# Kernel optimization log

Hardware: AMD Instinct MI355X
Metric: run time of the kernel (lower is better)

The kernel has to match this reference:

```python
import jax, jax.numpy as jnp
import numpy as np

P = 256          # planes == in_planes
EPS = 1e-5       # BatchNorm eps


def binarize(x):
    # sign with sign(0) -> +1, as in standard binary-net quantizers
    return jnp.where(x >= 0, 1.0, -1.0).astype(x.dtype)


def bin_conv(x, w, stride=1):
    """XNOR-style binarized 3x3 conv: sign(x) * sign(w), scaled by per-out-channel mean |w|."""
    ba = binarize(x)
    bw = binarize(w)
    scale = jnp.mean(jnp.abs(w), axis=(1, 2, 3))  # [O]
    y = jax.lax.conv_general_dilated(
        ba, bw, window_strides=(stride, stride), padding=((1, 1), (1, 1)),
        dimension_numbers=("NCHW", "OIHW", "NCHW"))
    return y * scale[None, :, None, None]


def bn(x, gamma, beta, mean, var):
    # inference-mode BatchNorm2d
    inv = gamma / jnp.sqrt(var + EPS)
    return x * inv[None, :, None, None] + (beta - mean * inv)[None, :, None, None]


def channel_shuffle(x, groups=2):
    b, c, h, w = x.shape
    return x.reshape(b, groups, c // groups, h, w).transpose(0, 2, 1, 3, 4).reshape(b, c, h, w)


def setup_inputs() -> dict:
    key = jax.random.key(0)
    ks = jax.random.split(key, 8)
    B, H, W = 16, 56, 56
    return {
        "x": jax.random.normal(ks[0], (B, 2 * P, H, W), jnp.float32),
        "w1": jax.random.normal(ks[1], (P, P, 3, 3), jnp.float32) * 0.05,
        "w2": jax.random.normal(ks[2], (P, 2 * P, 3, 3), jnp.float32) * 0.05,
        "gamma1": jnp.ones((P,), jnp.float32),
        "beta1": jnp.zeros((P,), jnp.float32),
        "mean1": jax.random.normal(ks[3], (P,), jnp.float32) * 0.1,
        "var1": jax.random.uniform(ks[4], (P,), jnp.float32) + 0.5,
        "gamma2": jnp.ones((P,), jnp.float32),
        "beta2": jnp.zeros((P,), jnp.float32),
        "mean2": jax.random.normal(ks[5], (P,), jnp.float32) * 0.1,
        "var2": jax.random.uniform(ks[6], (P,), jnp.float32) + 0.5,
        "move_bias": jax.random.normal(ks[7], (1, P, 1, 1), jnp.float32) * 0.1,
    }


def reference(x, w1, w2, gamma1, beta1, mean1, var1,
              gamma2, beta2, mean2, var2, move_bias):
    x_act, x_idle = x[:, :P], x[:, P:]
    residual = x_act
    out = bn(bin_conv(x_act, w1, stride=1), gamma1, beta1, mean1, var1)
    out = out + residual
    out = jnp.clip(out, -1.0, 1.0)            # Hardtanh
    x_idle = x_idle + move_bias               # LearnableBias
    out = jnp.concatenate([out, x_idle], axis=1)   # [B, 2P, H, W]
    out = channel_shuffle(out, groups=2)
    residual1 = out[:, :P]
    out = bn(bin_conv(out, w2, stride=1), gamma2, beta2, mean2, var2)
    out = out + residual1
    out = jnp.clip(out, -1.0, 1.0)            # Hardtanh
    return out
```

## Files before the change

### kernel.cpp

```cpp
#include <hip/hip_runtime.h>
#include <cstdint>

typedef unsigned long long u64;
typedef unsigned short u16;

#define HWSZ 3136
#define WD 56
#define NPIX 50176

__device__ __forceinline__ float clampf(float v){ return fminf(1.0f, fmaxf(-1.0f, v)); }

__global__ __launch_bounds__(256) void k_wprep(
    const float* __restrict__ w1, const float* __restrict__ w2,
    const float* __restrict__ g1, const float* __restrict__ be1,
    const float* __restrict__ m1, const float* __restrict__ v1,
    const float* __restrict__ g2, const float* __restrict__ be2,
    const float* __restrict__ m2, const float* __restrict__ v2,
    u64* __restrict__ w1b, u64* __restrict__ w2e, u64* __restrict__ w2o,
    float* __restrict__ A1, float* __restrict__ B1,
    float* __restrict__ A2, float* __restrict__ B2)
{
    int co  = blockIdx.x;
    int tid = threadIdx.x;
    int wv = tid >> 6, lane = tid & 63;
    int ci = (wv << 6) + lane;

    float s1 = 0.f, s2 = 0.f;
    const float* w1p = w1 + ((size_t)co * 256 + ci) * 9;
#pragma unroll
    for (int t = 0; t < 9; t++) {
        float v = w1p[t];
        s1 += fabsf(v);
        u64 bal = __ballot(v >= 0.f);
        if (lane == 0) w1b[(co * 9 + t) * 4 + wv] = bal;
    }
    const float* wep = w2 + ((size_t)co * 512 + 2 * ci) * 9;
    const float* wop = wep + 9;
#pragma unroll
    for (int t = 0; t < 9; t++) {
        float ve = wep[t], vo = wop[t];
        s2 += fabsf(ve) + fabsf(vo);
        u64 bale = __ballot(ve >= 0.f);
        u64 balo = __ballot(vo >= 0.f);
        if (lane == 0) { w2e[(co * 9 + t) * 4 + wv] = bale; w2o[(co * 9 + t) * 4 + wv] = balo; }
    }
    __shared__ float red1[256], red2[256];
    red1[tid] = s1; red2[tid] = s2;
    __syncthreads();
    for (int off = 128; off > 0; off >>= 1) {
        if (tid < off) { red1[tid] += red1[tid + off]; red2[tid] += red2[tid + off]; }
        __syncthreads();
    }
    if (tid == 0) {
        float scale1 = red1[0] / 2304.f;
        float scale2 = red2[0] / 4608.f;
        float inv1 = g1[co] / sqrtf(v1[co] + 1e-5f);
        float inv2 = g2[co] / sqrtf(v2[co] + 1e-5f);
        A1[co] = scale1 * inv1;  B1[co] = be1[co] - m1[co] * inv1;
        A2[co] = scale2 * inv2;  B2[co] = be2[co] - m2[co] * inv2;
    }
}

__global__ __launch_bounds__(256) void k_pack(
    const float* __restrict__ x, const float* __restrict__ mb,
    u64* __restrict__ bitsA, u64* __restrict__ bitsI)
{
    int tid = threadIdx.x;
    int p = blockIdx.x * 256 + tid;
    int q = blockIdx.y;
    int b = p / HWSZ, hw = p % HWSZ;
    const float* xa = x + ((size_t)(b * 512 + q * 64)) * HWSZ + hw;
    const float* xi = x + ((size_t)(b * 512 + 256 + q * 64)) * HWSZ + hw;
    const float* mbq = mb + q * 64;
    u64 wa = 0, wi = 0;
#pragma unroll 8
    for (int j = 0; j < 64; j++) {
        float va = xa[(size_t)j * HWSZ];
        float vi = xi[(size_t)j * HWSZ] + mbq[j];
        wa |= (u64)(va >= 0.f) << j;
        wi |= (u64)(vi >= 0.f) << j;
    }
    bitsA[(size_t)p * 4 + q] = wa;
    bitsI[(size_t)p * 4 + q] = wi;
}

__global__ __launch_bounds__(256, 4) void k_conv1(
    const float* __restrict__ x, const u64* __restrict__ bitsA,
    const u64* __restrict__ w1b, const float* __restrict__ A1, const float* __restrict__ B1,
    u64* __restrict__ bitsC, float* __restrict__ c1v)
{
    __shared__ u64 sw[2304];
    __shared__ float sA[64], sB[64];
    __shared__ u16 spart[4][128];
    int tid = threadIdx.x;
    int q = blockIdx.y;
    int cobase = q * 64;
    {
        const u64* src = w1b + (size_t)cobase * 36;
#pragma unroll
        for (int i = 0; i < 9; i++) sw[tid + i * 256] = src[tid + i * 256];
        if (tid < 64) { sA[tid] = A1[cobase + tid]; sB[tid] = B1[cobase + tid]; }
    }
    __syncthreads();

    int g = tid >> 6, lane = tid & 63;
    int pix0 = blockIdx.x * 128 + lane * 2;
    int b = pix0 / HWSZ, hw = pix0 % HWSZ;
    int h = hw / WD, w = hw % WD;

    int acc[16][2];
#pragma unroll
    for (int co = 0; co < 16; co++) { acc[co][0] = 0; acc[co][1] = 0; }
    int nv0 = 0, nv1 = 0;

#pragma unroll 1
    for (int dy = -1; dy <= 1; dy++) {
        bool rowok = ((unsigned)(h + dy)) < (unsigned)WD;
        u64 cb[4][4];
        int m[4];
#pragma unroll
        for (int k = 0; k < 4; k++) {
            int c = w - 1 + k;
            bool ok = rowok && ((unsigned)c < (unsigned)WD);
            int pg = pix0 + dy * WD + (k - 1);
            pg = pg < 0 ? 0 : (pg > NPIX - 1 ? NPIX - 1 : pg);
            const ulonglong2* pb = (const ulonglong2*)(bitsA + (size_t)pg * 4);
            ulonglong2 b01 = pb[0], b23 = pb[1];
            cb[k][0] = b01.x; cb[k][1] = b01.y; cb[k][2] = b23.x; cb[k][3] = b23.y;
            m[k] = ok ? -1 : 0;
        }
        int tbase = (dy + 1) * 3;
#pragma unroll
        for (int dx = 0; dx < 3; dx++) {
            int t = tbase + dx;
            nv0 -= m[dx]; nv1 -= m[dx + 1];
#pragma unroll
            for (int co = 0; co < 16; co++) {
                const u64* wp = &sw[(((g << 4) + co) * 9 + t) * 4];
                u64 w0 = wp[0], w1_ = wp[1], w2_ = wp[2], w3_ = wp[3];
#pragma unroll
                for (int p = 0; p < 2; p++) {
                    int k = dx + p;
                    int pt = __popcll(cb[k][0] ^ w0) + __popcll(cb[k][1] ^ w1_)
                           + __popcll(cb[k][2] ^ w2_) + __popcll(cb[k][3] ^ w3_);
                    acc[co][p] += pt & m[k];
                }
            }
        }
    }

    unsigned sb0 = 0, sb1 = 0;
    bool wr = (q < 2);
#pragma unroll
    for (int co = 0; co < 16; co++) {
        int col = (g << 4) + co;
        int coG = cobase + col;
        float A = sA[col], B = sB[col];
        float2 xr = *(const float2*)(x + (size_t)(b * 512 + coG) * HWSZ + hw);
        float v0 = (float)((nv0 << 8) - 2 * acc[co][0]) * A + B + xr.x;
        float v1 = (float)((nv1 << 8) - 2 * acc[co][1]) * A + B + xr.y;
        sb0 |= (unsigned)(v0 >= 0.f) << co;
        sb1 |= (unsigned)(v1 >= 0.f) << co;
        if (wr) {
            *(float2*)(c1v + (size_t)coG * NPIX + pix0) = make_float2(clampf(v0), clampf(v1));
        }
    }
    spart[g][lane * 2]     = (u16)sb0;
    spart[g][lane * 2 + 1] = (u16)sb1;
    __syncthreads();
    if (g == 0) {
#pragma unroll
        for (int p = 0; p < 2; p++) {
            int pi = lane * 2 + p;
            u64 word = (u64)spart[0][pi] | ((u64)spart[1][pi] << 16)
                     | ((u64)spart[2][pi] << 32) | ((u64)spart[3][pi] << 48);
            bitsC[(size_t)(pix0 + p) * 4 + q] = word;
        }
    }
}

__global__ __launch_bounds__(256, 3) void k_conv2(
    const float* __restrict__ x, const float* __restrict__ mb,
    const u64* __restrict__ bitsC, const u64* __restrict__ bitsI,
    const u64* __restrict__ w2e, const u64* __restrict__ w2o,
    const float* __restrict__ A2, const float* __restrict__ B2,
    const float* __restrict__ c1v, float* __restrict__ out)
{
    __shared__ u64 se[2304], so[2304];
    __shared__ float sA[64], sB[64], sM[32];
    int tid = threadIdx.x;
    int q = blockIdx.y;
    int cobase = q * 64;
    {
        const u64* srcE = w2e + (size_t)cobase * 36;
        const u64* srcO = w2o + (size_t)cobase * 36;
#pragma unroll
        for (int i = 0; i < 9; i++) { se[tid + i * 256] = srcE[tid + i * 256]; so[tid + i * 256] = srcO[tid + i * 256]; }
        if (tid < 64) { sA[tid] = A2[cobase + tid]; sB[tid] = B2[cobase + tid]; }
        if (tid < 32) { sM[tid] = mb[q * 32 + tid]; }
    }
    __syncthreads();

    int g = tid >> 6, lane = tid & 63;
    int pix0 = blockIdx.x * 128 + lane * 2;
    int b = pix0 / HWSZ, hw = pix0 % HWSZ;
    int h = hw / WD, w = hw % WD;

    int acc[16][2];
#pragma unroll
    for (int co = 0; co < 16; co++) { acc[co][0] = 0; acc[co][1] = 0; }
    int nv0 = 0, nv1 = 0;

#pragma unroll 1
    for (int dy = -1; dy <= 1; dy++) {
        bool rowok = ((unsigned)(h + dy)) < (unsigned)WD;
        u64 cb[4][4], ib[4][4];
        int m[4];
#pragma unroll
        for (int k = 0; k < 4; k++) {
            int c = w - 1 + k;
            bool ok = rowok && ((unsigned)c < (unsigned)WD);
            int pg = pix0 + dy * WD + (k - 1);
            pg = pg < 0 ? 0 : (pg > NPIX - 1 ? NPIX - 1 : pg);
            const ulonglong2* pc = (const ulonglong2*)(bitsC + (size_t)pg * 4);
            const ulonglong2* pi = (const ulonglong2*)(bitsI + (size_t)pg * 4);
            ulonglong2 c01 = pc[0], c23 = pc[1];
            ulonglong2 i01 = pi[0], i23 = pi[1];
            cb[k][0] = c01.x; cb[k][1] = c01.y; cb[k][2] = c23.x; cb[k][3] = c23.y;
            ib[k][0] = i01.x; ib[k][1] = i01.y; ib[k][2] = i23.x; ib[k][3] = i23.y;
            m[k] = ok ? -1 : 0;
        }
        int tbase = (dy + 1) * 3;
#pragma unroll
        for (int dx = 0; dx < 3; dx++) {
            int t = tbase + dx;
            nv0 -= m[dx]; nv1 -= m[dx + 1];
#pragma unroll
            for (int co = 0; co < 16; co++) {
                const u64* we = &se[(((g << 4) + co) * 9 + t) * 4];
                const u64* wo = &so[(((g << 4) + co) * 9 + t) * 4];
                u64 e0 = we[0], e1 = we[1], e2 = we[2], e3 = we[3];
                u64 o0 = wo[0], o1 = wo[1], o2 = wo[2], o3 = wo[3];
#pragma unroll
                for (int p = 0; p < 2; p++) {
                    int k = dx + p;
                    int pt = __popcll(cb[k][0] ^ e0) + __popcll(cb[k][1] ^ e1)
                           + __popcll(cb[k][2] ^ e2) + __popcll(cb[k][3] ^ e3)
                           + __popcll(ib[k][0] ^ o0) + __popcll(ib[k][1] ^ o1)
                           + __popcll(ib[k][2] ^ o2) + __popcll(ib[k][3] ^ o3);
                    acc[co][p] += pt & m[k];
                }
            }
        }
    }

#pragma unroll
    for (int co = 0; co < 16; co++) {
        int col = (g << 4) + co;
        int coG = cobase + col;
        int cg2 = coG >> 1;
        float A = sA[col], B = sB[col];
        float v0 = (float)((nv0 << 9) - 2 * acc[co][0]) * A + B;
        float v1 = (float)((nv1 << 9) - 2 * acc[co][1]) * A + B;
        float r0, r1;
        if ((co & 1) == 0) {
            float2 cv = *(const float2*)(c1v + (size_t)cg2 * NPIX + pix0);
            r0 = cv.x; r1 = cv.y;
        } else {
            float2 xi = *(const float2*)(x + (size_t)(b * 512 + 256 + cg2) * HWSZ + hw);
            float mbv = sM[col >> 1];
            r0 = xi.x + mbv; r1 = xi.y + mbv;
        }
        *(float2*)(out + (size_t)(b * 256 + coG) * HWSZ + hw) =
            make_float2(clampf(v0 + r0), clampf(v1 + r1));
    }
}

extern "C" void kernel_launch(void* const* d_in, const int* in_sizes, int n_in,
                              void* d_out, int out_size, void* d_ws, size_t ws_size,
                              hipStream_t stream)
{
    const float* x   = (const float*)d_in[0];
    const float* w1  = (const float*)d_in[1];
    const float* w2  = (const float*)d_in[2];
    const float* g1  = (const float*)d_in[3];
    const float* be1 = (const float*)d_in[4];
    const float* m1  = (const float*)d_in[5];
    const float* v1  = (const float*)d_in[6];
    const float* g2  = (const float*)d_in[7];
    const float* be2 = (const float*)d_in[8];
    const float* m2  = (const float*)d_in[9];
    const float* v2  = (const float*)d_in[10];
    const float* mb  = (const float*)d_in[11];

    char* ws = (char*)d_ws;
    u64* w1b = (u64*)ws; ws += 73728;
    u64* w2e = (u64*)ws; ws += 73728;
    u64* w2o = (u64*)ws; ws += 73728;
    float* A1 = (float*)ws; ws += 1024;
    float* B1 = (float*)ws; ws += 1024;
    float* A2 = (float*)ws; ws += 1024;
    float* B2 = (float*)ws; ws += 1024;
    u64* bitsA = (u64*)ws; ws += (size_t)NPIX * 4 * 8;
    u64* bitsI = (u64*)ws; ws += (size_t)NPIX * 4 * 8;
    u64* bitsC = (u64*)ws; ws += (size_t)NPIX * 4 * 8;
    float* c1v = (float*)ws; ws += (size_t)128 * NPIX * 4;

    hipLaunchKernelGGL(k_wprep, dim3(256), dim3(256), 0, stream,
                       w1, w2, g1, be1, m1, v1, g2, be2, m2, v2,
                       w1b, w2e, w2o, A1, B1, A2, B2);
    hipLaunchKernelGGL(k_pack, dim3(196, 4), dim3(256), 0, stream, x, mb, bitsA, bitsI);
    hipLaunchKernelGGL(k_conv1, dim3(392, 4), dim3(256), 0, stream,
                       x, bitsA, w1b, A1, B1, bitsC, c1v);
    hipLaunchKernelGGL(k_conv2, dim3(392, 4), dim3(256), 0, stream,
                       x, mb, bitsC, bitsI, w2e, w2o, A2, B2, c1v, (float*)d_out);
}
```

Before: 409.8 us.

## Process four pixels per thread in binary convs and store intermediate as bf16

Each thread now computes four adjacent output pixels instead of two, so the six loaded neighbour bit-words and each shared-memory weight load are reused across more popcounts, and the grid halves. Conv2 splits its active and idle halves into two sequential passes to limit register pressure, and the valid-tap counts are computed in closed form. The clamped conv1 residual buffer is written and read as bf16 instead of fp32, halving that traffic but adding rounding error to the residual. Occupancy hint for conv1 drops from 4 to 3 waves per SIMD, and the larger accumulator arrays raise register use.

```diff
diff --git a/kernel.cpp b/kernel.cpp
--- a/kernel.cpp
+++ b/kernel.cpp
@@ -9,6 +9,11 @@
 #define NPIX 50176
 
 __device__ __forceinline__ float clampf(float v){ return fminf(1.0f, fmaxf(-1.0f, v)); }
+__device__ __forceinline__ u16 f2bf(float f){
+    unsigned u = __float_as_uint(f);
+    return (u16)((u + 0x7fffu + ((u >> 16) & 1u)) >> 16);
+}
+__device__ __forceinline__ float bf2f(u16 h){ return __uint_as_float(((unsigned)h) << 16); }
 
 __global__ __launch_bounds__(256) void k_wprep(
     const float* __restrict__ w1, const float* __restrict__ w2,
@@ -84,14 +89,14 @@
     bitsI[(size_t)p * 4 + q] = wi;
 }
 
-__global__ __launch_bounds__(256, 4) void k_conv1(
+__global__ __launch_bounds__(256, 3) void k_conv1(
     const float* __restrict__ x, const u64* __restrict__ bitsA,
     const u64* __restrict__ w1b, const float* __restrict__ A1, const float* __restrict__ B1,
-    u64* __restrict__ bitsC, float* __restrict__ c1v)
+    u64* __restrict__ bitsC, u16* __restrict__ c1v)
 {
     __shared__ u64 sw[2304];
     __shared__ float sA[64], sB[64];
-    __shared__ u16 spart[4][128];
+    __shared__ u16 spart[4][256];
     int tid = threadIdx.x;
     int q = blockIdx.y;
     int cobase = q * 64;
@@ -104,74 +109,89 @@
     __syncthreads();
 
     int g = tid >> 6, lane = tid & 63;
-    int pix0 = blockIdx.x * 128 + lane * 2;
+    int pix0 = blockIdx.x * 256 + lane * 4;
     int b = pix0 / HWSZ, hw = pix0 % HWSZ;
     int h = hw / WD, w = hw % WD;
 
-    int acc[16][2];
-#pragma unroll
-    for (int co = 0; co < 16; co++) { acc[co][0] = 0; acc[co][1] = 0; }
-    int nv0 = 0, nv1 = 0;
+    int acc[16][4];
+#pragma unroll
+    for (int co = 0; co < 16; co++)
+#pragma unroll
+        for (int p = 0; p < 4; p++) acc[co][p] = 0;
 
 #pragma unroll 1
     for (int dy = -1; dy <= 1; dy++) {
         bool rowok = ((unsigned)(h + dy)) < (unsigned)WD;
-        u64 cb[4][4];
-        int m[4];
-#pragma unroll
-        for (int k = 0; k < 4; k++) {
+        u64 pos[6][4];
+        int m[6];
+#pragma unroll
+        for (int k = 0; k < 6; k++) {
             int c = w - 1 + k;
             bool ok = rowok && ((unsigned)c < (unsigned)WD);
             int pg = pix0 + dy * WD + (k - 1);
             pg = pg < 0 ? 0 : (pg > NPIX - 1 ? NPIX - 1 : pg);
             const ulonglong2* pb = (const ulonglong2*)(bitsA + (size_t)pg * 4);
-            ulonglong2 b01 = pb[0], b23 = pb[1];
-            cb[k][0] = b01.x; cb[k][1] = b01.y; cb[k][2] = b23.x; cb[k][3] = b23.y;
+            ulonglong2 a01 = pb[0], a23 = pb[1];
+            pos[k][0] = a01.x; pos[k][1] = a01.y; pos[k][2] = a23.x; pos[k][3] = a23.y;
             m[k] = ok ? -1 : 0;
         }
         int tbase = (dy + 1) * 3;
 #pragma unroll
         for (int dx = 0; dx < 3; dx++) {
             int t = tbase + dx;
-            nv0 -= m[dx]; nv1 -= m[dx + 1];
 #pragma unroll
             for (int co = 0; co < 16; co++) {
                 const u64* wp = &sw[(((g << 4) + co) * 9 + t) * 4];
                 u64 w0 = wp[0], w1_ = wp[1], w2_ = wp[2], w3_ = wp[3];
 #pragma unroll
-                for (int p = 0; p < 2; p++) {
+                for (int p = 0; p < 4; p++) {
                     int k = dx + p;
-                    int pt = __popcll(cb[k][0] ^ w0) + __popcll(cb[k][1] ^ w1_)
-                           + __popcll(cb[k][2] ^ w2_) + __popcll(cb[k][3] ^ w3_);
+                    int pt = __popcll(pos[k][0] ^ w0) + __popcll(pos[k][1] ^ w1_)
+                           + __popcll(pos[k][2] ^ w2_) + __popcll(pos[k][3] ^ w3_);
                     acc[co][p] += pt & m[k];
                 }
             }
         }
     }
 
-    unsigned sb0 = 0, sb1 = 0;
+    int rowsv = 3 - (h == 0) - (h == WD - 1);
+    int nv[4];
+#pragma unroll
+    for (int p = 0; p < 4; p++) {
+        int wp_ = w + p;
+        nv[p] = rowsv * (3 - (wp_ == 0) - (wp_ == WD - 1));
+    }
+
+    unsigned sb[4] = {0, 0, 0, 0};
     bool wr = (q < 2);
 #pragma unroll
     for (int co = 0; co < 16; co++) {
         int col = (g << 4) + co;
         int coG = cobase + col;
         float A = sA[col], B = sB[col];
-        float2 xr = *(const float2*)(x + (size_t)(b * 512 + coG) * HWSZ + hw);
-        float v0 = (float)((nv0 << 8) - 2 * acc[co][0]) * A + B + xr.x;
-        float v1 = (float)((nv1 << 8) - 2 * acc[co][1]) * A + B + xr.y;
-        sb0 |= (unsigned)(v0 >= 0.f) << co;
-        sb1 |= (unsigned)(v1 >= 0.f) << co;
+        float4 xr = *(const float4*)(x + (size_t)(b * 512 + coG) * HWSZ + hw);
+        float v0 = (float)((nv[0] << 8) - 2 * acc[co][0]) * A + B + xr.x;
+        float v1 = (float)((nv[1] << 8) - 2 * acc[co][1]) * A + B + xr.y;
+        float v2 = (float)((nv[2] << 8) - 2 * acc[co][2]) * A + B + xr.z;
+        float v3 = (float)((nv[3] << 8) - 2 * acc[co][3]) * A + B + xr.w;
+        sb[0] |= (unsigned)(v0 >= 0.f) << co;
+        sb[1] |= (unsigned)(v1 >= 0.f) << co;
+        sb[2] |= (unsigned)(v2 >= 0.f) << co;
+        sb[3] |= (unsigned)(v3 >= 0.f) << co;
         if (wr) {
-            *(float2*)(c1v + (size_t)coG * NPIX + pix0) = make_float2(clampf(v0), clampf(v1));
-        }
-    }
-    spart[g][lane * 2]     = (u16)sb0;
-    spart[g][lane * 2 + 1] = (u16)sb1;
+            ushort4 st;
+            st.x = f2bf(clampf(v0)); st.y = f2bf(clampf(v1));
+            st.z = f2bf(clampf(v2)); st.w = f2bf(clampf(v3));
+            *(ushort4*)(c1v + (size_t)coG * NPIX + pix0) = st;
+        }
+    }
+#pragma unroll
+    for (int p = 0; p < 4; p++) spart[g][lane * 4 + p] = (u16)sb[p];
     __syncthreads();
     if (g == 0) {
 #pragma unroll
-        for (int p = 0; p < 2; p++) {
-            int pi = lane * 2 + p;
+        for (int p = 0; p < 4; p++) {
+            int pi = lane * 4 + p;
             u64 word = (u64)spart[0][pi] | ((u64)spart[1][pi] << 16)
                      | ((u64)spart[2][pi] << 32) | ((u64)spart[3][pi] << 48);
             bitsC[(size_t)(pix0 + p) * 4 + q] = word;
@@ -184,7 +204,7 @@
     const u64* __restrict__ bitsC, const u64* __restrict__ bitsI,
     const u64* __restrict__ w2e, const u64* __restrict__ w2o,
     const float* __restrict__ A2, const float* __restrict__ B2,
-    const float* __restrict__ c1v, float* __restrict__ out)
+    const u16* __restrict__ c1v, float* __restrict__ out)
 {
     __shared__ u64 se[2304], so[2304];
     __shared__ float sA[64], sB[64], sM[32];
@@ -202,56 +222,62 @@
     __syncthreads();
 
     int g = tid >> 6, lane = tid & 63;
-    int pix0 = blockIdx.x * 128 + lane * 2;
+    int pix0 = blockIdx.x * 256 + lane * 4;
     int b = pix0 / HWSZ, hw = pix0 % HWSZ;
     int h = hw / WD, w = hw % WD;
 
-    int acc[16][2];
-#pragma unroll
-    for (int co = 0; co < 16; co++) { acc[co][0] = 0; acc[co][1] = 0; }
-    int nv0 = 0, nv1 = 0;
+    int acc[16][4];
+#pragma unroll
+    for (int co = 0; co < 16; co++)
+#pragma unroll
+        for (int p = 0; p < 4; p++) acc[co][p] = 0;
 
 #pragma unroll 1
-    for (int dy = -1; dy <= 1; dy++) {
-        bool rowok = ((unsigned)(h + dy)) < (unsigned)WD;
-        u64 cb[4][4], ib[4][4];
-        int m[4];
-#pragma unroll
-        for (int k = 0; k < 4; k++) {
-            int c = w - 1 + k;
-            bool ok = rowok && ((unsigned)c < (unsigned)WD);
-            int pg = pix0 + dy * WD + (k - 1);
-            pg = pg < 0 ? 0 : (pg > NPIX - 1 ? NPIX - 1 : pg);
-            const ulonglong2* pc = (const ulonglong2*)(bitsC + (size_t)pg * 4);
-            const ulonglong2* pi = (const ulonglong2*)(bitsI + (size_t)pg * 4);
-            ulonglong2 c01 = pc[0], c23 = pc[1];
-            ulonglong2 i01 = pi[0], i23 = pi[1];
-            cb[k][0] = c01.x; cb[k][1] = c01.y; cb[k][2] = c23.x; cb[k][3] = c23.y;
-            ib[k][0] = i01.x; ib[k][1] = i01.y; ib[k][2] = i23.x; ib[k][3] = i23.y;
-            m[k] = ok ? -1 : 0;
-        }
-        int tbase = (dy + 1) * 3;
-#pragma unroll
-        for (int dx = 0; dx < 3; dx++) {
-            int t = tbase + dx;
-            nv0 -= m[dx]; nv1 -= m[dx + 1];
-#pragma unroll
-            for (int co = 0; co < 16; co++) {
-                const u64* we = &se[(((g << 4) + co) * 9 + t) * 4];
-                const u64* wo = &so[(((g << 4) + co) * 9 + t) * 4];
-                u64 e0 = we[0], e1 = we[1], e2 = we[2], e3 = we[3];
-                u64 o0 = wo[0], o1 = wo[1], o2 = wo[2], o3 = wo[3];
-#pragma unroll
-                for (int p = 0; p < 2; p++) {
-                    int k = dx + p;
-                    int pt = __popcll(cb[k][0] ^ e0) + __popcll(cb[k][1] ^ e1)
-                           + __popcll(cb[k][2] ^ e2) + __popcll(cb[k][3] ^ e3)
-                           + __popcll(ib[k][0] ^ o0) + __popcll(ib[k][1] ^ o1)
-                           + __popcll(ib[k][2] ^ o2) + __popcll(ib[k][3] ^ o3);
-                    acc[co][p] += pt & m[k];
+    for (int pass = 0; pass < 2; pass++) {
+        const u64* bits = pass ? bitsI : bitsC;
+        const u64* swp  = pass ? so : se;
+#pragma unroll 1
+        for (int dy = -1; dy <= 1; dy++) {
+            bool rowok = ((unsigned)(h + dy)) < (unsigned)WD;
+            u64 pos[6][4];
+            int m[6];
+#pragma unroll
+            for (int k = 0; k < 6; k++) {
+                int c = w - 1 + k;
+                bool ok = rowok && ((unsigned)c < (unsigned)WD);
+                int pg = pix0 + dy * WD + (k - 1);
+                pg = pg < 0 ? 0 : (pg > NPIX - 1 ? NPIX - 1 : pg);
+                const ulonglong2* pb = (const ulonglong2*)(bits + (size_t)pg * 4);
+                ulonglong2 a01 = pb[0], a23 = pb[1];
+                pos[k][0] = a01.x; pos[k][1] = a01.y; pos[k][2] = a23.x; pos[k][3] = a23.y;
+                m[k] = ok ? -1 : 0;
+            }
+            int tbase = (dy + 1) * 3;
+#pragma unroll
+            for (int dx = 0; dx < 3; dx++) {
+                int t = tbase + dx;
+#pragma unroll
+                for (int co = 0; co < 16; co++) {
+                    const u64* wp = &swp[(((g << 4) + co) * 9 + t) * 4];
+                    u64 w0 = wp[0], w1_ = wp[1], w2_ = wp[2], w3_ = wp[3];
+#pragma unroll
+                    for (int p = 0; p < 4; p++) {
+                        int k = dx + p;
+                        int pt = __popcll(pos[k][0] ^ w0) + __popcll(pos[k][1] ^ w1_)
+                               + __popcll(pos[k][2] ^ w2_) + __popcll(pos[k][3] ^ w3_);
+                        acc[co][p] += pt & m[k];
+                    }
                 }
             }
         }
+    }
+
+    int rowsv = 3 - (h == 0) - (h == WD - 1);
+    int nv[4];
+#pragma unroll
+    for (int p = 0; p < 4; p++) {
+        int wp_ = w + p;
+        nv[p] = rowsv * (3 - (wp_ == 0) - (wp_ == WD - 1));
     }
 
 #pragma unroll
@@ -260,19 +286,21 @@
         int coG = cobase + col;
         int cg2 = coG >> 1;
         float A = sA[col], B = sB[col];
-        float v0 = (float)((nv0 << 9) - 2 * acc[co][0]) * A + B;
-        float v1 = (float)((nv1 << 9) - 2 * acc[co][1]) * A + B;
-        float r0, r1;
+        float r0, r1, r2, r3;
         if ((co & 1) == 0) {
-            float2 cv = *(const float2*)(c1v + (size_t)cg2 * NPIX + pix0);
-            r0 = cv.x; r1 = cv.y;
+            ushort4 cv = *(const ushort4*)(c1v + (size_t)cg2 * NPIX + pix0);
+            r0 = bf2f(cv.x); r1 = bf2f(cv.y); r2 = bf2f(cv.z); r3 = bf2f(cv.w);
         } else {
-            float2 xi = *(const float2*)(x + (size_t)(b * 512 + 256 + cg2) * HWSZ + hw);
+            float4 xi = *(const float4*)(x + (size_t)(b * 512 + 256 + cg2) * HWSZ + hw);
             float mbv = sM[col >> 1];
-            r0 = xi.x + mbv; r1 = xi.y + mbv;
-        }
-        *(float2*)(out + (size_t)(b * 256 + coG) * HWSZ + hw) =
-            make_float2(clampf(v0 + r0), clampf(v1 + r1));
+            r0 = xi.x + mbv; r1 = xi.y + mbv; r2 = xi.z + mbv; r3 = xi.w + mbv;
+        }
+        float4 ov;
+        ov.x = clampf((float)((nv[0] << 9) - 2 * acc[co][0]) * A + B + r0);
+        ov.y = clampf((float)((nv[1] << 9) - 2 * acc[co][1]) * A + B + r1);
+        ov.z = clampf((float)((nv[2] << 9) - 2 * acc[co][2]) * A + B + r2);
+        ov.w = clampf((float)((nv[3] << 9) - 2 * acc[co][3]) * A + B + r3);
+        *(float4*)(out + (size_t)(b * 256 + coG) * HWSZ + hw) = ov;
     }
 }
 
@@ -304,14 +332,14 @@
     u64* bitsA = (u64*)ws; ws += (size_t)NPIX * 4 * 8;
     u64* bitsI = (u64*)ws; ws += (size_t)NPIX * 4 * 8;
     u64* bitsC = (u64*)ws; ws += (size_t)NPIX * 4 * 8;
-    float* c1v = (float*)ws; ws += (size_t)128 * NPIX * 4;
+    u16* c1v = (u16*)ws; ws += (size_t)128 * NPIX * 2;
 
     hipLaunchKernelGGL(k_wprep, dim3(256), dim3(256), 0, stream,
                        w1, w2, g1, be1, m1, v1, g2, be2, m2, v2,
                        w1b, w2e, w2o, A1, B1, A2, B2);
     hipLaunchKernelGGL(k_pack, dim3(196, 4), dim3(256), 0, stream, x, mb, bitsA, bitsI);
-    hipLaunchKernelGGL(k_conv1, dim3(392, 4), dim3(256), 0, stream,
+    hipLaunchKernelGGL(k_conv1, dim3(196, 4), dim3(256), 0, stream,
                        x, bitsA, w1b, A1, B1, bitsC, c1v);
-    hipLaunchKernelGGL(k_conv2, dim3(392, 4), dim3(256), 0, stream,
+    hipLaunchKernelGGL(k_conv2, dim3(196, 4), dim3(256), 0, stream,
                        x, mb, bitsC, bitsI, w2e, w2o, A2, B2, c1v, (float*)d_out);
 }
```

Measured after the change: 479.4 us. 17.0% more time.
